# Kernel optimization log

Hardware: AMD Instinct MI355X
Metric: run time of the kernel (lower is better)

Reference implementation:

```python
import jax, jax.numpy as jnp
import numpy as np
from jax.scipy.special import logsumexp

# Special-tag indices (module-level globals in the original repo)
PAD_IDX, SOS_IDX, EOS_IDX = 0, 1, 2
NEG = -10000.0


def setup_inputs() -> dict:
    L, B, T = 1024, 2048, 16
    key = jax.random.key(0)
    k1, k2, k3, k4 = jax.random.split(key, 4)
    h = jax.random.normal(k1, (L, B, T), dtype=jnp.float32)
    y0 = jax.random.randint(k2, (L + 1, B), 0, T)  # gold tag path, [L+1, B]
    # prefix-of-ones mask from random lengths in [L//2, L]
    lengths = jax.random.randint(k4, (B,), L // 2, L + 1)
    mask = (jnp.arange(L)[:, None] < lengths[None, :]).astype(jnp.float32)
    # transition matrix, init as in CRF.__init__
    trans = jax.random.normal(k3, (T, T), dtype=jnp.float32) * 0.01
    trans = (trans.at[SOS_IDX, :].set(NEG)
                  .at[:, EOS_IDX].set(NEG)
                  .at[:, PAD_IDX].set(NEG)
                  .at[PAD_IDX, :].set(NEG)
                  .at[PAD_IDX, EOS_IDX].set(0.0)
                  .at[PAD_IDX, PAD_IDX].set(0.0))
    return {"h": h, "y0": y0, "mask": mask, "trans": trans}


def _crf_loss(h, y0, mask, trans):
    L, B, T = h.shape
    # ---- score(h, y0, mask): note original uses _emit = 0 (emissions unused here)
    # S[b] = sum_t trans[y0[t+1,b], y0[t,b]] * mask[t,b]  for t in [0, L-2]
    S = jnp.sum(trans[y0[1:L], y0[: L - 1]] * mask[: L - 1], axis=0)  # [B]
    lengths = jnp.sum(mask, axis=0).astype(jnp.int32)                  # [B]
    last_tag = y0[lengths, jnp.arange(B)]                              # [B]
    S = S + trans[PAD_IDX, last_tag]

    # ---- partition(h, mask): forward algorithm over sigmoid(h)
    hs = jax.nn.sigmoid(h)
    Z0 = jnp.full((B, T), NEG, dtype=h.dtype).at[:, SOS_IDX].set(0.0)

    def step(Z, xm):
        _h, _m = xm                                   # [B,T], [B]
        # _Z[b,i] = logsumexp_j( Z[b,j] + _h[b,i] + trans[i,j] )
        _Z = logsumexp(Z[:, None, :] + _h[:, :, None] + trans[None, :, :], axis=2)
        Z = _Z * _m[:, None] + Z * (1.0 - _m[:, None])
        return Z, None

    Z, _ = jax.lax.scan(step, Z0, (hs, mask))
    Z = logsumexp(Z + trans[EOS_IDX], axis=1)         # [B]

    return jnp.mean(Z - S)


def reference(h, y0, mask, trans):
    return _crf_loss(h, y0, mask, trans)
```

## Files before the change

kernel.cpp:

```cpp
#include <hip/hip_runtime.h>


typedef unsigned int u32;
typedef float f32x4 __attribute__((ext_vector_type(4)));
typedef short s16x4 __attribute__((ext_vector_type(4)));
typedef unsigned int u32x2 __attribute__((ext_vector_type(2)));

#define LOG2E 1.4426950408889634f
#define LN2   0.6931471805599453f
#define Bsz   2048
#define Lsz   1024
#define BT    32768
#define GSTR  20

#if __has_builtin(__builtin_amdgcn_exp2f)
__device__ __forceinline__ float exp2x(float x){ return __builtin_amdgcn_exp2f(x); }
#else
__device__ __forceinline__ float exp2x(float x){ return exp2f(x); }
#endif
#if __has_builtin(__builtin_amdgcn_logf)
__device__ __forceinline__ float log2x(float x){ return __builtin_amdgcn_logf(x); }
#else
__device__ __forceinline__ float log2x(float x){ return log2f(x); }
#endif
#if __has_builtin(__builtin_amdgcn_rcpf)
__device__ __forceinline__ float rcpx(float x){ return __builtin_amdgcn_rcpf(x); }
#else
__device__ __forceinline__ float rcpx(float x){ return 1.0f/x; }
#endif

__device__ __forceinline__ u32 cvtpk_bf16(float lo, float hi){
  u32 r;
  asm("v_cvt_pk_bf16_f32 %0, %1, %2" : "=v"(r) : "v"(lo), "v"(hi));
  return r;
}

__device__ __forceinline__ f32x4 mfma16(s16x4 a, s16x4 b, f32x4 c){
  f32x4 d;
  asm volatile("s_nop 1\n\t"
      "v_mfma_f32_16x16x16_bf16 %0, %1, %2, %3\n\t"
      "s_nop 7\n\t"
      "s_nop 7"
      : "=&v"(d) : "v"(a), "v"(b), "v"(c));
  return d;
}

__global__ __launch_bounds__(256) void k_zero(float* lenw, float* Sw, float* out){
  int i = blockIdx.x*256 + threadIdx.x;
  if (i < Bsz) lenw[i] = 0.f;
  else if (i < 2*Bsz) Sw[i - Bsz] = 0.f;
  if (i == 0) out[0] = 0.f;
}

__global__ __launch_bounds__(256) void k_score(const int* __restrict__ y0,
    const float* __restrict__ mask, const float* __restrict__ trans,
    float* __restrict__ lenw, float* __restrict__ Sw){
  __shared__ float Tt[256];
  Tt[threadIdx.x] = trans[threadIdx.x];
  __syncthreads();
  int gid = blockIdx.x*256 + threadIdx.x;
  int b  = gid & (Bsz-1);
  int tc = gid >> 11;
  int t0 = tc * 32;
  float lacc = 0.f, sacc = 0.f;
  int yc = y0[t0*Bsz + b];
  #pragma unroll 4
  for (int t = t0; t < t0+32; ++t) {
    float m = mask[t*Bsz + b];
    int yn = y0[(t+1)*Bsz + b];
    lacc += m;
    if (t <= Lsz-2) sacc += m * Tt[yn*16 + yc];
    yc = yn;
  }
  atomicAdd(&lenw[b], lacc);
  atomicAdd(&Sw[b], sacc);
}

__global__ __launch_bounds__(256) void k_phase1(const float* __restrict__ h,
    const float* __restrict__ trans, const float* __restrict__ lenw,
    u32x2* __restrict__ Pout){
  __shared__ __align__(16) float gbuf[4][65*GSTR];
  int warp = threadIdx.x >> 6;
  int wid  = blockIdx.x*4 + warp;
  int c    = wid >> 11;
  int b    = wid & (Bsz-1);
  int lane = threadIdx.x & 63;
  int cl   = lane & 15;
  int grp  = lane >> 4;
  int t0   = c << 6;
  int len  = (int)(lenw[b] + 0.5f);
  int active = len - t0;
  if (active <= 0) return;
  if (active > 64) active = 64;

  {
    const float* hp = h + (size_t)(t0 + grp)*BT + b*16 + cl;
    float* wp = &gbuf[warp][0];
    #pragma unroll
    for (int i = 0; i < 16; ++i) {
      float hv = hp[(size_t)(4*i)*BT];
      float sg = rcpx(1.f + exp2x(hv * (-LOG2E)));
      wp[(4*i + grp)*GSTR + cl] = exp2x(sg * LOG2E);
    }
  }

  union { u32 u[2]; s16x4 v; } EA;
  {
    const float* tp = trans + cl*16 + grp*4;
    float E0 = exp2x(tp[0]*LOG2E) * 0.0625f;
    float E1 = exp2x(tp[1]*LOG2E) * 0.0625f;
    float E2 = exp2x(tp[2]*LOG2E) * 0.0625f;
    float E3 = exp2x(tp[3]*LOG2E) * 0.0625f;
    EA.u[0] = cvtpk_bf16(E0, E1);
    EA.u[1] = cvtpk_bf16(E2, E3);
  }

  int k0 = grp*4;
  u32 bx = ((k0+0)==cl ? 0x3F80u : 0u) | (((k0+1)==cl ? 0x3F80u : 0u) << 16);
  u32 by = ((k0+2)==cl ? 0x3F80u : 0u) | (((k0+3)==cl ? 0x3F80u : 0u) << 16);
  const f32x4 z4 = {0.f, 0.f, 0.f, 0.f};

  const float* gp = &gbuf[warp][grp*4];

  f32x4 gc = *(const f32x4*)(gp);
  #pragma unroll 2
  for (int s = 0; s < active; ++s) {
    f32x4 gn = *(const f32x4*)(gp + (s+1)*GSTR);
    union { u32 u[2]; s16x4 v; } Bf;
    Bf.u[0] = bx; Bf.u[1] = by;
    f32x4 d = mfma16(EA.v, Bf.v, z4);
    float v0 = d.x*gc.x, v1 = d.y*gc.y;
    float v2 = d.z*gc.z, v3 = d.w*gc.w;
    bx = cvtpk_bf16(v0, v1);
    by = cvtpk_bf16(v2, v3);
    gc = gn;
  }

  Pout[(size_t)(b*16 + c)*64 + lane] = (u32x2){bx, by};
}

__global__ __launch_bounds__(256) void k_phase2(const u32x2* __restrict__ P,
    const float* __restrict__ trans, const float* __restrict__ lenw,
    const float* __restrict__ Sw, const int* __restrict__ y0,
    float* __restrict__ out){
  __shared__ float red[4];
  int b = blockIdx.x*4 + (threadIdx.x >> 6);
  int lane = threadIdx.x & 63;
  int cl = lane & 15, grp = lane >> 4;
  int len = (int)(lenw[b] + 0.5f);
  float v = (cl == 1) ? 1.f : 0.f;
  float lsc = 0.f;
  int nch = (len + 63) >> 6;
  const u32x2* Pb = P + (size_t)b*16*64;
  int srcaddr = (cl >> 2) << 6;
  int msel = cl & 3;
  for (int c = 0; c < nch; ++c) {
    u32x2 pw = Pb[c*64 + lane];
    float p0 = __uint_as_float(pw.x << 16);
    float p1 = __uint_as_float(pw.x & 0xffff0000u);
    float p2 = __uint_as_float(pw.y << 16);
    float p3 = __uint_as_float(pw.y & 0xffff0000u);
    float q0 = p0*v, q1 = p1*v, q2 = p2*v, q3 = p3*v;
    #pragma unroll
    for (int mk = 1; mk <= 8; mk <<= 1) {
      q0 += __shfl_xor(q0, mk);
      q1 += __shfl_xor(q1, mk);
      q2 += __shfl_xor(q2, mk);
      q3 += __shfl_xor(q3, mk);
    }
    float t0v = __int_as_float(__builtin_amdgcn_ds_bpermute(srcaddr, __float_as_int(q0)));
    float t1v = __int_as_float(__builtin_amdgcn_ds_bpermute(srcaddr, __float_as_int(q1)));
    float t2v = __int_as_float(__builtin_amdgcn_ds_bpermute(srcaddr, __float_as_int(q2)));
    float t3v = __int_as_float(__builtin_amdgcn_ds_bpermute(srcaddr, __float_as_int(q3)));
    float vn = (msel==0) ? t0v : (msel==1) ? t1v : (msel==2) ? t2v : t3v;
    float gm = fmaxf(fmaxf(q0,q1), fmaxf(q2,q3));
    gm = fmaxf(gm, __shfl_xor(gm, 16));
    gm = fmaxf(gm, __shfl_xor(gm, 32));
    int eb = (int)((__float_as_uint(gm) >> 23) & 0xff) - 127;
    float sc = __uint_as_float((u32)(127 - eb) << 23);
    v = vn * sc;
    lsc += (float)eb;
  }
  float eE = exp2x(trans[32 + cl] * LOG2E);
  float num = v * eE;
  num += __shfl_xor(num, 1);
  num += __shfl_xor(num, 2);
  num += __shfl_xor(num, 4);
  num += __shfl_xor(num, 8);
  if (lane == 0) {
    float Z = (log2x(num) + lsc + 4.f*(float)len) * LN2;
    int lastTag = y0[(size_t)len*Bsz + b];
    float Sb = Sw[b] + trans[lastTag];
    red[threadIdx.x >> 6] = (Z - Sb) * (1.f/(float)Bsz);
  }
  __syncthreads();
  if (threadIdx.x == 0) {
    atomicAdd(out, red[0] + red[1] + red[2] + red[3]);
  }
}

extern "C" void kernel_launch(void* const* d_in, const int* in_sizes, int n_in,
                              void* d_out, int out_size, void* d_ws, size_t ws_size,
                              hipStream_t stream) {
  const float* h     = (const float*)d_in[0];
  const int*   y0    = (const int*)d_in[1];
  const float* mask  = (const float*)d_in[2];
  const float* trans = (const float*)d_in[3];
  float* out  = (float*)d_out;
  float* lenw = (float*)d_ws;
  float* Sw   = lenw + Bsz;
  u32x2* P    = (u32x2*)((char*)d_ws + 16384);

  k_zero  <<<16,   256, 0, stream>>>(lenw, Sw, out);
  k_score <<<256,  256, 0, stream>>>(y0, mask, trans, lenw, Sw);
  k_phase1<<<8192, 256, 0, stream>>>(h, trans, lenw, P);
  k_phase2<<<512,  256, 0, stream>>>(P, trans, lenw, Sw, y0, out);
}
```

Before: 87.24 us.

## Interleave two chunk recurrences per wave with hand-written MFMA asm loop

Each wave now processes two 64-step chunks (one from the first half of the sequence, one from the second) and interleaves their independent MFMA chains in a hand-scheduled inline-asm loop. The goal is to hide MFMA latency, which the single dependent chain left exposed. Gate values are stored as packed bf16 in LDS and loaded with float2 reads, which halves LDS traffic, and the grid is halved. In exchange the code hard-codes VGPRs in inline asm, handles odd step counts with a tail step, and adds more bf16 rounding of the gate factors.

```diff
diff --git a/kernel.cpp b/kernel.cpp
--- a/kernel.cpp
+++ b/kernel.cpp
@@ -11,7 +11,6 @@
 #define Bsz   2048
 #define Lsz   1024
 #define BT    32768
-#define GSTR  20
 
 #if __has_builtin(__builtin_amdgcn_exp2f)
 __device__ __forceinline__ float exp2x(float x){ return __builtin_amdgcn_exp2f(x); }
@@ -44,6 +43,89 @@
       : "=&v"(d) : "v"(a), "v"(b), "v"(c));
   return d;
 }
+
+#define RUN_SEG(CNT, A0, A1, B0X, B0Y, B1X, B1Y, ELO, EHI)                     \
+  asm volatile(                                                                \
+    "s_waitcnt lgkmcnt(0)\n\t"                                                 \
+    "v_mov_b32 v40, %[b0x]\n\t"                                                \
+    "v_mov_b32 v41, %[b0y]\n\t"                                                \
+    "v_mov_b32 v42, %[b1x]\n\t"                                                \
+    "v_mov_b32 v43, %[b1y]\n\t"                                                \
+    "v_mov_b32 v56, %[elo]\n\t"                                                \
+    "v_mov_b32 v57, %[ehi]\n\t"                                                \
+    "v_mov_b32 v58, 0\n\t"                                                     \
+    "v_mov_b32 v59, 0\n\t"                                                     \
+    "v_mov_b32 v60, 0\n\t"                                                     \
+    "v_mov_b32 v61, 0\n\t"                                                     \
+    ".LP%=:\n\t"                                                               \
+    "ds_read_b128 v[44:47], %[a0]\n\t"                                         \
+    "ds_read_b128 v[48:51], %[a1]\n\t"                                         \
+    "v_add_u32 %[a0], 16, %[a0]\n\t"                                           \
+    "v_add_u32 %[a1], 16, %[a1]\n\t"                                           \
+    "s_waitcnt lgkmcnt(0)\n\t"                                                 \
+    "s_nop 1\n\t"                                                              \
+    "v_mfma_f32_16x16x16_bf16 v[32:35], v[56:57], v[40:41], v[58:61]\n\t"      \
+    "v_mfma_f32_16x16x16_bf16 v[36:39], v[56:57], v[42:43], v[58:61]\n\t"      \
+    "v_lshlrev_b32 v52, 16, v44\n\t"                                           \
+    "v_and_b32 v53, 0xffff0000, v44\n\t"                                       \
+    "v_lshlrev_b32 v54, 16, v45\n\t"                                           \
+    "v_and_b32 v55, 0xffff0000, v45\n\t"                                       \
+    "s_nop 6\n\t"                                                              \
+    "v_mul_f32 v52, v32, v52\n\t"                                              \
+    "v_mul_f32 v53, v33, v53\n\t"                                              \
+    "v_mul_f32 v54, v34, v54\n\t"                                              \
+    "v_mul_f32 v55, v35, v55\n\t"                                              \
+    "v_cvt_pk_bf16_f32 v40, v52, v53\n\t"                                      \
+    "v_cvt_pk_bf16_f32 v41, v54, v55\n\t"                                      \
+    "v_lshlrev_b32 v52, 16, v48\n\t"                                           \
+    "v_and_b32 v53, 0xffff0000, v48\n\t"                                       \
+    "v_lshlrev_b32 v54, 16, v49\n\t"                                           \
+    "v_and_b32 v55, 0xffff0000, v49\n\t"                                       \
+    "v_mul_f32 v52, v36, v52\n\t"                                              \
+    "v_mul_f32 v53, v37, v53\n\t"                                              \
+    "v_mul_f32 v54, v38, v54\n\t"                                              \
+    "v_mul_f32 v55, v39, v55\n\t"                                              \
+    "v_cvt_pk_bf16_f32 v42, v52, v53\n\t"                                      \
+    "v_cvt_pk_bf16_f32 v43, v54, v55\n\t"                                      \
+    "s_nop 1\n\t"                                                              \
+    "v_mfma_f32_16x16x16_bf16 v[32:35], v[56:57], v[40:41], v[58:61]\n\t"      \
+    "v_mfma_f32_16x16x16_bf16 v[36:39], v[56:57], v[42:43], v[58:61]\n\t"      \
+    "v_lshlrev_b32 v52, 16, v46\n\t"                                           \
+    "v_and_b32 v53, 0xffff0000, v46\n\t"                                       \
+    "v_lshlrev_b32 v54, 16, v47\n\t"                                           \
+    "v_and_b32 v55, 0xffff0000, v47\n\t"                                       \
+    "s_nop 6\n\t"                                                              \
+    "v_mul_f32 v52, v32, v52\n\t"                                              \
+    "v_mul_f32 v53, v33, v53\n\t"                                              \
+    "v_mul_f32 v54, v34, v54\n\t"                                              \
+    "v_mul_f32 v55, v35, v55\n\t"                                              \
+    "v_cvt_pk_bf16_f32 v40, v52, v53\n\t"                                      \
+    "v_cvt_pk_bf16_f32 v41, v54, v55\n\t"                                      \
+    "v_lshlrev_b32 v52, 16, v50\n\t"                                           \
+    "v_and_b32 v53, 0xffff0000, v50\n\t"                                       \
+    "v_lshlrev_b32 v54, 16, v51\n\t"                                           \
+    "v_and_b32 v55, 0xffff0000, v51\n\t"                                       \
+    "v_mul_f32 v52, v36, v52\n\t"                                              \
+    "v_mul_f32 v53, v37, v53\n\t"                                              \
+    "v_mul_f32 v54, v38, v54\n\t"                                              \
+    "v_mul_f32 v55, v39, v55\n\t"                                              \
+    "v_cvt_pk_bf16_f32 v42, v52, v53\n\t"                                      \
+    "v_cvt_pk_bf16_f32 v43, v54, v55\n\t"                                      \
+    "s_sub_u32 %[cnt], %[cnt], 1\n\t"                                          \
+    "s_cmp_lg_u32 %[cnt], 0\n\t"                                               \
+    "s_cbranch_scc1 .LP%=\n\t"                                                 \
+    "v_mov_b32 %[b0x], v40\n\t"                                                \
+    "v_mov_b32 %[b0y], v41\n\t"                                                \
+    "v_mov_b32 %[b1x], v42\n\t"                                                \
+    "v_mov_b32 %[b1y], v43"                                                    \
+    : [a0]"+v"(A0), [a1]"+v"(A1), [cnt]"+s"(CNT),                              \
+      [b0x]"+v"(B0X), [b0y]"+v"(B0Y), [b1x]"+v"(B1X), [b1y]"+v"(B1Y)           \
+    : [elo]"v"(ELO), [ehi]"v"(EHI)                                             \
+    : "memory",                                                                \
+      "v32","v33","v34","v35","v36","v37","v38","v39",                         \
+      "v40","v41","v42","v43","v44","v45","v46","v47",                         \
+      "v48","v49","v50","v51","v52","v53","v54","v55",                         \
+      "v56","v57","v58","v59","v60","v61")
 
 __global__ __launch_bounds__(256) void k_zero(float* lenw, float* Sw, float* out){
   int i = blockIdx.x*256 + threadIdx.x;
@@ -79,64 +161,90 @@
 __global__ __launch_bounds__(256) void k_phase1(const float* __restrict__ h,
     const float* __restrict__ trans, const float* __restrict__ lenw,
     u32x2* __restrict__ Pout){
-  __shared__ __align__(16) float gbuf[4][65*GSTR];
+  __shared__ __align__(16) u32 gbuf[4][2][4*132];
   int warp = threadIdx.x >> 6;
   int wid  = blockIdx.x*4 + warp;
-  int c    = wid >> 11;
+  int cpair= wid >> 11;
   int b    = wid & (Bsz-1);
   int lane = threadIdx.x & 63;
   int cl   = lane & 15;
   int grp  = lane >> 4;
-  int t0   = c << 6;
   int len  = (int)(lenw[b] + 0.5f);
-  int active = len - t0;
-  if (active <= 0) return;
-  if (active > 64) active = 64;
+  int t0a  = cpair << 6;
+  int t0b  = 512 + (cpair << 6);
+  int a1   = len - t0b;
+  a1 = a1 < 0 ? 0 : (a1 > 64 ? 64 : a1);
 
   {
-    const float* hp = h + (size_t)(t0 + grp)*BT + b*16 + cl;
-    float* wp = &gbuf[warp][0];
+    int m = lane & 7, trow = lane >> 3;
     #pragma unroll
-    for (int i = 0; i < 16; ++i) {
-      float hv = hp[(size_t)(4*i)*BT];
-      float sg = rcpx(1.f + exp2x(hv * (-LOG2E)));
-      wp[(4*i + grp)*GSTR + cl] = exp2x(sg * LOG2E);
+    for (int cc = 0; cc < 2; ++cc) {
+      if (cc == 1 && a1 <= 0) break;
+      int tt0 = cc ? t0b : t0a;
+      const float* hp = h + (size_t)tt0*BT + b*16 + 2*m;
+      u32* wp = &gbuf[warp][cc][(m>>1)*132 + (m&1)];
+      #pragma unroll
+      for (int k = 0; k < 8; ++k) {
+        int t = trow + 8*k;
+        float2 hv = *(const float2*)&hp[(size_t)t*BT];
+        float g0 = exp2x(rcpx(1.f + exp2x(hv.x * (-LOG2E))) * LOG2E);
+        float g1 = exp2x(rcpx(1.f + exp2x(hv.y * (-LOG2E))) * LOG2E);
+        wp[2*t] = cvtpk_bf16(g0, g1);
+      }
     }
   }
 
-  union { u32 u[2]; s16x4 v; } EA;
+  u32 elo, ehi;
   {
     const float* tp = trans + cl*16 + grp*4;
     float E0 = exp2x(tp[0]*LOG2E) * 0.0625f;
     float E1 = exp2x(tp[1]*LOG2E) * 0.0625f;
     float E2 = exp2x(tp[2]*LOG2E) * 0.0625f;
     float E3 = exp2x(tp[3]*LOG2E) * 0.0625f;
-    EA.u[0] = cvtpk_bf16(E0, E1);
-    EA.u[1] = cvtpk_bf16(E2, E3);
+    elo = cvtpk_bf16(E0, E1);
+    ehi = cvtpk_bf16(E2, E3);
   }
 
   int k0 = grp*4;
-  u32 bx = ((k0+0)==cl ? 0x3F80u : 0u) | (((k0+1)==cl ? 0x3F80u : 0u) << 16);
-  u32 by = ((k0+2)==cl ? 0x3F80u : 0u) | (((k0+3)==cl ? 0x3F80u : 0u) << 16);
-  const f32x4 z4 = {0.f, 0.f, 0.f, 0.f};
-
-  const float* gp = &gbuf[warp][grp*4];
-
-  f32x4 gc = *(const f32x4*)(gp);
-  #pragma unroll 2
-  for (int s = 0; s < active; ++s) {
-    f32x4 gn = *(const f32x4*)(gp + (s+1)*GSTR);
-    union { u32 u[2]; s16x4 v; } Bf;
-    Bf.u[0] = bx; Bf.u[1] = by;
-    f32x4 d = mfma16(EA.v, Bf.v, z4);
-    float v0 = d.x*gc.x, v1 = d.y*gc.y;
-    float v2 = d.z*gc.z, v3 = d.w*gc.w;
-    bx = cvtpk_bf16(v0, v1);
-    by = cvtpk_bf16(v2, v3);
-    gc = gn;
-  }
-
-  Pout[(size_t)(b*16 + c)*64 + lane] = (u32x2){bx, by};
+  u32 ibx = ((k0+0)==cl ? 0x3F80u : 0u) | (((k0+1)==cl ? 0x3F80u : 0u) << 16);
+  u32 iby = ((k0+2)==cl ? 0x3F80u : 0u) | (((k0+3)==cl ? 0x3F80u : 0u) << 16);
+  u32 b0x = ibx, b0y = iby, b1x = ibx, b1y = iby;
+
+  u32 a0 = (u32)(unsigned long long)&gbuf[warp][0][grp*132];
+  u32 a1a= (u32)(unsigned long long)&gbuf[warp][1][grp*132];
+
+  int p = a1 >> 1;
+  int odd = a1 & 1;
+
+  if (p > 0) {
+    u32 cnt = (u32)__builtin_amdgcn_readfirstlane(p);
+    RUN_SEG(cnt, a0, a1a, b0x, b0y, b1x, b1y, elo, ehi);
+  }
+
+  if (odd) {
+    u32x2 gw = *(const u32x2*)&gbuf[warp][1][grp*132 + 4*p];
+    float f0 = __uint_as_float(gw.x << 16);
+    float f1 = __uint_as_float(gw.x & 0xffff0000u);
+    float f2 = __uint_as_float(gw.y << 16);
+    float f3 = __uint_as_float(gw.y & 0xffff0000u);
+    union { u32 u[2]; s16x4 v; } EAv, Bf;
+    EAv.u[0] = elo; EAv.u[1] = ehi;
+    Bf.u[0] = b1x; Bf.u[1] = b1y;
+    const f32x4 z4 = {0.f,0.f,0.f,0.f};
+    f32x4 d = mfma16(EAv.v, Bf.v, z4);
+    b1x = cvtpk_bf16(d.x*f0, d.y*f1);
+    b1y = cvtpk_bf16(d.z*f2, d.w*f3);
+  }
+  u32 p1x = b1x, p1y = b1y;
+
+  if (p < 32) {
+    u32 cnt = (u32)__builtin_amdgcn_readfirstlane(32 - p);
+    RUN_SEG(cnt, a0, a1a, b0x, b0y, b1x, b1y, elo, ehi);
+  }
+
+  Pout[(size_t)(b*16 + cpair)*64 + lane] = (u32x2){b0x, b0y};
+  if (a1 > 0)
+    Pout[(size_t)(b*16 + cpair + 8)*64 + lane] = (u32x2){p1x, p1y};
 }
 
 __global__ __launch_bounds__(256) void k_phase2(const u32x2* __restrict__ P,
@@ -213,6 +321,6 @@
 
   k_zero  <<<16,   256, 0, stream>>>(lenw, Sw, out);
   k_score <<<256,  256, 0, stream>>>(y0, mask, trans, lenw, Sw);
-  k_phase1<<<8192, 256, 0, stream>>>(h, trans, lenw, P);
+  k_phase1<<<4096, 256, 0, stream>>>(h, trans, lenw, P);
   k_phase2<<<512,  256, 0, stream>>>(P, trans, lenw, Sw, y0, out);
 }
```

New measurement: 91.20 us. 1.05x slower.

## Restructure phase1 chain into 4-step MFMA tree to cut serial latency

Applied to the files above, without the earlier changes.

Replaces the strictly serial per-step MFMA recurrence in phase1 with groups of four steps. Each group builds per-step transfer matrices (transposed and normal orientation with gate scaling) and combines them in a small tree of MFMAs, so the dependent chain per four steps is shorter. A scalar tail loop handles the remainder. This adds more MFMAs, conversions and hardcoded VGPR clobbers, and extra bf16 rounding of intermediate products could affect accuracy.

```diff
diff --git a/kernel.cpp b/kernel.cpp
--- a/kernel.cpp
+++ b/kernel.cpp
@@ -43,6 +43,37 @@
       "s_nop 7"
       : "=&v"(d) : "v"(a), "v"(b), "v"(c));
   return d;
+}
+
+__device__ __forceinline__ void tree4(s16x4 l0, s16x4 l1, s16x4 l2, s16x4 l3,
+                                      s16x4 vv, f32x4 z, u32& vo0, u32& vo1){
+  asm volatile(
+    "s_nop 1\n\t"
+    "v_mfma_f32_16x16x16_bf16 v[40:43], %[l0], %[l1], %[z]\n\t"
+    "v_mfma_f32_16x16x16_bf16 v[44:47], %[l2], %[l3], %[z]\n\t"
+    "s_nop 7\n\t"
+    "s_nop 7\n\t"
+    "v_cvt_pk_bf16_f32 v48, v40, v41\n\t"
+    "v_cvt_pk_bf16_f32 v49, v42, v43\n\t"
+    "s_nop 1\n\t"
+    "v_mfma_f32_16x16x16_bf16 v[40:43], v[48:49], %[vv], %[z]\n\t"
+    "v_cvt_pk_bf16_f32 v50, v44, v45\n\t"
+    "v_cvt_pk_bf16_f32 v51, v46, v47\n\t"
+    "s_nop 7\n\t"
+    "s_nop 3\n\t"
+    "v_cvt_pk_bf16_f32 v52, v40, v41\n\t"
+    "v_cvt_pk_bf16_f32 v53, v42, v43\n\t"
+    "s_nop 1\n\t"
+    "v_mfma_f32_16x16x16_bf16 v[44:47], v[50:51], v[52:53], %[z]\n\t"
+    "s_nop 7\n\t"
+    "s_nop 7\n\t"
+    "v_cvt_pk_bf16_f32 %[o0], v44, v45\n\t"
+    "v_cvt_pk_bf16_f32 %[o1], v46, v47"
+    : [o0]"=&v"(vo0), [o1]"=&v"(vo1)
+    : [l0]"v"(l0), [l1]"v"(l1), [l2]"v"(l2), [l3]"v"(l3),
+      [vv]"v"(vv), [z]"v"(z)
+    : "v40","v41","v42","v43","v44","v45","v46","v47",
+      "v48","v49","v50","v51","v52","v53");
 }
 
 __global__ __launch_bounds__(256) void k_zero(float* lenw, float* Sw, float* out){
@@ -104,36 +135,54 @@
     }
   }
 
-  union { u32 u[2]; s16x4 v; } EA;
+  int k0 = grp*4;
+  float EA0, EA1, EA2, EA3, EB0, EB1, EB2, EB3;
   {
-    const float* tp = trans + cl*16 + grp*4;
-    float E0 = exp2x(tp[0]*LOG2E) * 0.0625f;
-    float E1 = exp2x(tp[1]*LOG2E) * 0.0625f;
-    float E2 = exp2x(tp[2]*LOG2E) * 0.0625f;
-    float E3 = exp2x(tp[3]*LOG2E) * 0.0625f;
-    EA.u[0] = cvtpk_bf16(E0, E1);
-    EA.u[1] = cvtpk_bf16(E2, E3);
-  }
-
-  int k0 = grp*4;
+    const float* tpA = trans + cl*16 + k0;
+    EA0 = exp2x(tpA[0]*LOG2E) * 0.0625f;
+    EA1 = exp2x(tpA[1]*LOG2E) * 0.0625f;
+    EA2 = exp2x(tpA[2]*LOG2E) * 0.0625f;
+    EA3 = exp2x(tpA[3]*LOG2E) * 0.0625f;
+    EB0 = exp2x(trans[(k0+0)*16 + cl]*LOG2E) * 0.0625f;
+    EB1 = exp2x(trans[(k0+1)*16 + cl]*LOG2E) * 0.0625f;
+    EB2 = exp2x(trans[(k0+2)*16 + cl]*LOG2E) * 0.0625f;
+    EB3 = exp2x(trans[(k0+3)*16 + cl]*LOG2E) * 0.0625f;
+  }
+  union { u32 u[2]; s16x4 v; } EApk;
+  EApk.u[0] = cvtpk_bf16(EA0, EA1);
+  EApk.u[1] = cvtpk_bf16(EA2, EA3);
+
   u32 bx = ((k0+0)==cl ? 0x3F80u : 0u) | (((k0+1)==cl ? 0x3F80u : 0u) << 16);
   u32 by = ((k0+2)==cl ? 0x3F80u : 0u) | (((k0+3)==cl ? 0x3F80u : 0u) << 16);
   const f32x4 z4 = {0.f, 0.f, 0.f, 0.f};
-
-  const float* gp = &gbuf[warp][grp*4];
-
-  f32x4 gc = *(const f32x4*)(gp);
-  #pragma unroll 2
-  for (int s = 0; s < active; ++s) {
-    f32x4 gn = *(const f32x4*)(gp + (s+1)*GSTR);
+  const float* gp = &gbuf[warp][0];
+
+  int S = active >> 2;
+  for (int s = 0; s < S; ++s) {
+    int t = 4*s;
+    f32x4 g0 = *(const f32x4*)(gp + (t+0)*GSTR + k0);
+    float  s1 = gp[(t+1)*GSTR + cl];
+    f32x4 g2 = *(const f32x4*)(gp + (t+2)*GSTR + k0);
+    float  s3 = gp[(t+3)*GSTR + cl];
+    union { u32 u[2]; s16x4 v; } L0, L1, L2, L3, Vv;
+    L0.u[0] = cvtpk_bf16(EB0*g0.x, EB1*g0.y);
+    L0.u[1] = cvtpk_bf16(EB2*g0.z, EB3*g0.w);
+    L1.u[0] = cvtpk_bf16(EA0*s1, EA1*s1);
+    L1.u[1] = cvtpk_bf16(EA2*s1, EA3*s1);
+    L2.u[0] = cvtpk_bf16(EB0*g2.x, EB1*g2.y);
+    L2.u[1] = cvtpk_bf16(EB2*g2.z, EB3*g2.w);
+    L3.u[0] = cvtpk_bf16(EA0*s3, EA1*s3);
+    L3.u[1] = cvtpk_bf16(EA2*s3, EA3*s3);
+    Vv.u[0] = bx; Vv.u[1] = by;
+    tree4(L0.v, L1.v, L2.v, L3.v, Vv.v, z4, bx, by);
+  }
+  for (int s = 4*S; s < active; ++s) {
+    f32x4 g4 = *(const f32x4*)(gp + s*GSTR + k0);
     union { u32 u[2]; s16x4 v; } Bf;
     Bf.u[0] = bx; Bf.u[1] = by;
-    f32x4 d = mfma16(EA.v, Bf.v, z4);
-    float v0 = d.x*gc.x, v1 = d.y*gc.y;
-    float v2 = d.z*gc.z, v3 = d.w*gc.w;
-    bx = cvtpk_bf16(v0, v1);
-    by = cvtpk_bf16(v2, v3);
-    gc = gn;
+    f32x4 d = mfma16(EApk.v, Bf.v, z4);
+    bx = cvtpk_bf16(d.x*g4.x, d.y*g4.y);
+    by = cvtpk_bf16(d.z*g4.z, d.w*g4.w);
   }
 
   Pout[(size_t)(b*16 + c)*64 + lane] = (u32x2){bx, by};
```

Result: faster. 84.51 us (-3.1%).

## Fuse chunked CRF forward into single sequential chain kernel with producer warps

Applied to the files above, without the earlier changes.

Replaces the two-phase chunked scheme (per-chunk transfer-matrix products, then a combine pass) with one kernel per 16 batch elements. In each block, three warps stream sigmoid-exp emissions into double-buffered LDS as bf16, and one warp runs the full 1024-step recurrence with a single MFMA per step, renormalising once per window. This removes the 16x16 matrix-product work and the intermediate P buffer round trip. In exchange, parallelism drops to 128 blocks, each with a single serial consumer warp over the whole sequence, so the dependent chain runs 1024 steps long.

```diff
diff --git a/kernel.cpp b/kernel.cpp
--- a/kernel.cpp
+++ b/kernel.cpp
@@ -11,7 +11,7 @@
 #define Bsz   2048
 #define Lsz   1024
 #define BT    32768
-#define GSTR  20
+#define RS    132
 
 #if __has_builtin(__builtin_amdgcn_exp2f)
 __device__ __forceinline__ float exp2x(float x){ return __builtin_amdgcn_exp2f(x); }
@@ -76,126 +76,106 @@
   atomicAdd(&Sw[b], sacc);
 }
 
-__global__ __launch_bounds__(256) void k_phase1(const float* __restrict__ h,
-    const float* __restrict__ trans, const float* __restrict__ lenw,
-    u32x2* __restrict__ Pout){
-  __shared__ __align__(16) float gbuf[4][65*GSTR];
-  int warp = threadIdx.x >> 6;
-  int wid  = blockIdx.x*4 + warp;
-  int c    = wid >> 11;
-  int b    = wid & (Bsz-1);
-  int lane = threadIdx.x & 63;
-  int cl   = lane & 15;
-  int grp  = lane >> 4;
-  int t0   = c << 6;
-  int len  = (int)(lenw[b] + 0.5f);
-  int active = len - t0;
-  if (active <= 0) return;
-  if (active > 64) active = 64;
 
-  {
-    const float* hp = h + (size_t)(t0 + grp)*BT + b*16 + cl;
-    float* wp = &gbuf[warp][0];
-    #pragma unroll
-    for (int i = 0; i < 16; ++i) {
-      float hv = hp[(size_t)(4*i)*BT];
-      float sg = rcpx(1.f + exp2x(hv * (-LOG2E)));
-      wp[(4*i + grp)*GSTR + cl] = exp2x(sg * LOG2E);
+__device__ __forceinline__ void produce_win(int win, u32* __restrict__ dst,
+    const float* __restrict__ hp, int warp){
+  #pragma unroll
+  for (int k = 0; k < 11; ++k) {
+    int r = 3*k + warp;
+    if (r < 32) {
+      int t = (win << 5) + r;
+      f32x4 hv = *(const f32x4*)(hp + (size_t)t*BT);
+      float g0 = exp2x(rcpx(1.f + exp2x(hv.x * (-LOG2E))) * LOG2E);
+      float g1 = exp2x(rcpx(1.f + exp2x(hv.y * (-LOG2E))) * LOG2E);
+      float g2 = exp2x(rcpx(1.f + exp2x(hv.z * (-LOG2E))) * LOG2E);
+      float g3 = exp2x(rcpx(1.f + exp2x(hv.w * (-LOG2E))) * LOG2E);
+      u32x2 pk; pk.x = cvtpk_bf16(g0, g1); pk.y = cvtpk_bf16(g2, g3);
+      *(u32x2*)&dst[r*RS] = pk;
     }
   }
-
-  union { u32 u[2]; s16x4 v; } EA;
-  {
-    const float* tp = trans + cl*16 + grp*4;
-    float E0 = exp2x(tp[0]*LOG2E) * 0.0625f;
-    float E1 = exp2x(tp[1]*LOG2E) * 0.0625f;
-    float E2 = exp2x(tp[2]*LOG2E) * 0.0625f;
-    float E3 = exp2x(tp[3]*LOG2E) * 0.0625f;
-    EA.u[0] = cvtpk_bf16(E0, E1);
-    EA.u[1] = cvtpk_bf16(E2, E3);
-  }
-
-  int k0 = grp*4;
-  u32 bx = ((k0+0)==cl ? 0x3F80u : 0u) | (((k0+1)==cl ? 0x3F80u : 0u) << 16);
-  u32 by = ((k0+2)==cl ? 0x3F80u : 0u) | (((k0+3)==cl ? 0x3F80u : 0u) << 16);
-  const f32x4 z4 = {0.f, 0.f, 0.f, 0.f};
-
-  const float* gp = &gbuf[warp][grp*4];
-
-  f32x4 gc = *(const f32x4*)(gp);
-  #pragma unroll 2
-  for (int s = 0; s < active; ++s) {
-    f32x4 gn = *(const f32x4*)(gp + (s+1)*GSTR);
-    union { u32 u[2]; s16x4 v; } Bf;
-    Bf.u[0] = bx; Bf.u[1] = by;
-    f32x4 d = mfma16(EA.v, Bf.v, z4);
-    float v0 = d.x*gc.x, v1 = d.y*gc.y;
-    float v2 = d.z*gc.z, v3 = d.w*gc.w;
-    bx = cvtpk_bf16(v0, v1);
-    by = cvtpk_bf16(v2, v3);
-    gc = gn;
-  }
-
-  Pout[(size_t)(b*16 + c)*64 + lane] = (u32x2){bx, by};
 }
 
-__global__ __launch_bounds__(256) void k_phase2(const u32x2* __restrict__ P,
+__global__ __launch_bounds__(256) void k_chain(const float* __restrict__ h,
     const float* __restrict__ trans, const float* __restrict__ lenw,
     const float* __restrict__ Sw, const int* __restrict__ y0,
     float* __restrict__ out){
-  __shared__ float red[4];
-  int b = blockIdx.x*4 + (threadIdx.x >> 6);
+  __shared__ __align__(16) u32 gwin[2][32*RS];
+  int warp = threadIdx.x >> 6;
   int lane = threadIdx.x & 63;
-  int cl = lane & 15, grp = lane >> 4;
-  int len = (int)(lenw[b] + 0.5f);
-  float v = (cl == 1) ? 1.f : 0.f;
-  float lsc = 0.f;
-  int nch = (len + 63) >> 6;
-  const u32x2* Pb = P + (size_t)b*16*64;
-  int srcaddr = (cl >> 2) << 6;
-  int msel = cl & 3;
-  for (int c = 0; c < nch; ++c) {
-    u32x2 pw = Pb[c*64 + lane];
-    float p0 = __uint_as_float(pw.x << 16);
-    float p1 = __uint_as_float(pw.x & 0xffff0000u);
-    float p2 = __uint_as_float(pw.y << 16);
-    float p3 = __uint_as_float(pw.y & 0xffff0000u);
-    float q0 = p0*v, q1 = p1*v, q2 = p2*v, q3 = p3*v;
-    #pragma unroll
-    for (int mk = 1; mk <= 8; mk <<= 1) {
-      q0 += __shfl_xor(q0, mk);
-      q1 += __shfl_xor(q1, mk);
-      q2 += __shfl_xor(q2, mk);
-      q3 += __shfl_xor(q3, mk);
+  int b0   = blockIdx.x << 4;
+  int cl   = lane & 15, grp = lane >> 4;
+
+  int pb = lane >> 2, pq = lane & 3;
+  const float* hp = h + (size_t)(b0 + pb)*16 + 4*pq;
+  int pcell = pb*8 + pq*2;
+
+  union { u32 u[2]; s16x4 v; } EApk;
+  {
+    const float* tp = trans + cl*16 + grp*4;
+    EApk.u[0] = cvtpk_bf16(exp2x(tp[0]*LOG2E)*0.0625f, exp2x(tp[1]*LOG2E)*0.0625f);
+    EApk.u[1] = cvtpk_bf16(exp2x(tp[2]*LOG2E)*0.0625f, exp2x(tp[3]*LOG2E)*0.0625f);
+  }
+  f32x4 v4 = {0.f, (grp == 0) ? 1.f : 0.f, 0.f, 0.f};
+  int   lenc = (int)(lenw[b0 + cl] + 0.5f);
+  float lsc  = 0.f;
+  const f32x4 z4 = {0.f, 0.f, 0.f, 0.f};
+  int ccell = cl*8 + grp*2;
+
+  if (warp < 3) produce_win(0, &gwin[0][pcell], hp, warp);
+  __syncthreads();
+
+  for (int win = 0; win < 32; ++win) {
+    if (warp < 3) {
+      if (win + 1 < 32) produce_win(win + 1, &gwin[(win + 1) & 1][pcell], hp, warp);
+    } else {
+      const u32* src = &gwin[win & 1][ccell];
+      int tbase = win << 5;
+      #pragma unroll 4
+      for (int r = 0; r < 32; ++r) {
+        u32x2 gg = *(const u32x2*)&src[r*RS];
+        union { u32 u[2]; s16x4 v; } Bf;
+        Bf.u[0] = cvtpk_bf16(v4.x, v4.y);
+        Bf.u[1] = cvtpk_bf16(v4.z, v4.w);
+        f32x4 dn = mfma16(EApk.v, Bf.v, z4);
+        float g0 = __uint_as_float(gg.x << 16);
+        float g1 = __uint_as_float(gg.x & 0xffff0000u);
+        float g2 = __uint_as_float(gg.y << 16);
+        float g3 = __uint_as_float(gg.y & 0xffff0000u);
+        bool live = (tbase + r) < lenc;
+        v4.x = live ? dn.x*g0 : v4.x;
+        v4.y = live ? dn.y*g1 : v4.y;
+        v4.z = live ? dn.z*g2 : v4.z;
+        v4.w = live ? dn.w*g3 : v4.w;
+      }
+      float mx = fmaxf(fmaxf(v4.x, v4.y), fmaxf(v4.z, v4.w));
+      mx = fmaxf(mx, __shfl_xor(mx, 16));
+      mx = fmaxf(mx, __shfl_xor(mx, 32));
+      int eb = (int)((__float_as_uint(mx) >> 23) & 0xff) - 127;
+      float sc = __uint_as_float((u32)(127 - eb) << 23);
+      v4.x *= sc; v4.y *= sc; v4.z *= sc; v4.w *= sc;
+      lsc += (float)eb;
     }
-    float t0v = __int_as_float(__builtin_amdgcn_ds_bpermute(srcaddr, __float_as_int(q0)));
-    float t1v = __int_as_float(__builtin_amdgcn_ds_bpermute(srcaddr, __float_as_int(q1)));
-    float t2v = __int_as_float(__builtin_amdgcn_ds_bpermute(srcaddr, __float_as_int(q2)));
-    float t3v = __int_as_float(__builtin_amdgcn_ds_bpermute(srcaddr, __float_as_int(q3)));
-    float vn = (msel==0) ? t0v : (msel==1) ? t1v : (msel==2) ? t2v : t3v;
-    float gm = fmaxf(fmaxf(q0,q1), fmaxf(q2,q3));
-    gm = fmaxf(gm, __shfl_xor(gm, 16));
-    gm = fmaxf(gm, __shfl_xor(gm, 32));
-    int eb = (int)((__float_as_uint(gm) >> 23) & 0xff) - 127;
-    float sc = __uint_as_float((u32)(127 - eb) << 23);
-    v = vn * sc;
-    lsc += (float)eb;
+    __syncthreads();
   }
-  float eE = exp2x(trans[32 + cl] * LOG2E);
-  float num = v * eE;
-  num += __shfl_xor(num, 1);
-  num += __shfl_xor(num, 2);
-  num += __shfl_xor(num, 4);
-  num += __shfl_xor(num, 8);
-  if (lane == 0) {
-    float Z = (log2x(num) + lsc + 4.f*(float)len) * LN2;
-    int lastTag = y0[(size_t)len*Bsz + b];
-    float Sb = Sw[b] + trans[lastTag];
-    red[threadIdx.x >> 6] = (Z - Sb) * (1.f/(float)Bsz);
-  }
-  __syncthreads();
-  if (threadIdx.x == 0) {
-    atomicAdd(out, red[0] + red[1] + red[2] + red[3]);
+
+  if (warp == 3) {
+    const float* te = trans + 32 + grp*4;
+    float p = v4.x*exp2x(te[0]*LOG2E) + v4.y*exp2x(te[1]*LOG2E)
+            + v4.z*exp2x(te[2]*LOG2E) + v4.w*exp2x(te[3]*LOG2E);
+    p += __shfl_xor(p, 16);
+    p += __shfl_xor(p, 32);
+    float contrib = 0.f;
+    if (grp == 0) {
+      float Z = (log2x(p) + lsc + 4.f*(float)lenc) * LN2;
+      int lastTag = y0[(size_t)lenc*Bsz + (b0 + cl)];
+      float Sb = Sw[b0 + cl] + trans[lastTag];
+      contrib = (Z - Sb) * (1.f/2048.f);
+    }
+    contrib += __shfl_xor(contrib, 1);
+    contrib += __shfl_xor(contrib, 2);
+    contrib += __shfl_xor(contrib, 4);
+    contrib += __shfl_xor(contrib, 8);
+    if (lane == 0) atomicAdd(out, contrib);
   }
 }
 
@@ -209,10 +189,8 @@
   float* out  = (float*)d_out;
   float* lenw = (float*)d_ws;
   float* Sw   = lenw + Bsz;
-  u32x2* P    = (u32x2*)((char*)d_ws + 16384);
 
-  k_zero  <<<16,   256, 0, stream>>>(lenw, Sw, out);
-  k_score <<<256,  256, 0, stream>>>(y0, mask, trans, lenw, Sw);
-  k_phase1<<<8192, 256, 0, stream>>>(h, trans, lenw, P);
-  k_phase2<<<512,  256, 0, stream>>>(P, trans, lenw, Sw, y0, out);
+  k_zero  <<<16,  256, 0, stream>>>(lenw, Sw, out);
+  k_score <<<256, 256, 0, stream>>>(y0, mask, trans, lenw, Sw);
+  k_chain <<<128, 256, 0, stream>>>(h, trans, lenw, Sw, y0, out);
 }
```

After: 109.2 us. 25.1% more time.
